# Kernel tuning notes

Hardware: AMD Instinct MI355X
Metric: run time of the kernel (lower is better)

The kernel has to match this reference:

```python
import math
import jax, jax.numpy as jnp
import numpy as np

ALPHA = 1000.0
N_LAMBDA = 1.0


def setup_inputs() -> dict:
    key = jax.random.key(0)
    k1, k2 = jax.random.split(key)
    xyz1 = jax.random.normal(k1, (4, 8192, 3), dtype=jnp.float32)  # prediction
    xyz2 = jax.random.normal(k2, (4, 8192, 3), dtype=jnp.float32)  # ground truth
    return {"xyz1": xyz1, "xyz2": xyz2}


def _nn(a, b):
    """For each point in a [B,Na,3], squared dist + index of nearest point in b [B,Nb,3]."""
    a2 = jnp.sum(a * a, axis=-1)[:, :, None]          # [B,Na,1]
    b2 = jnp.sum(b * b, axis=-1)[:, None, :]          # [B,1,Nb]
    d = a2 + b2 - 2.0 * jnp.einsum('bnd,bmd->bnm', a, b)  # [B,Na,Nb]
    return jnp.min(d, axis=-1), jnp.argmin(d, axis=-1)


def reference(xyz1, xyz2):
    B, n_x, _ = xyz1.shape
    n_gt = xyz2.shape[1]
    frac_21 = n_gt / n_x

    # torch code calls ChamferFunction.apply(xyz2, xyz1):
    # dist1/idx1 are for gt points (idx1 indexes into xyz1, range n_x),
    # dist2/idx2 are for pred points (idx2 indexes into xyz2, range n_gt).
    dist1, idx1 = _nn(xyz2, xyz1)   # [B, n_gt]
    dist2, idx2 = _nn(xyz1, xyz2)   # [B, n_x]

    exp_dist1 = jnp.exp(-dist1 * ALPHA)
    exp_dist2 = jnp.exp(-dist2 * ALPHA)

    batch = jnp.arange(B)[:, None]

    # how many gt points picked each pred point
    count1 = jnp.zeros((B, n_x), jnp.int32).at[batch, idx1].add(1)
    weight1 = jnp.take_along_axis(count1, idx1, axis=1).astype(jnp.float32) ** N_LAMBDA
    weight1 = 1.0 / jnp.maximum(frac_21 / weight1 + 1e-6, 1.0)
    loss1 = jnp.mean(1.0 - exp_dist1 * weight1, axis=1)

    # how many pred points picked each gt point
    count2 = jnp.zeros((B, n_gt), jnp.int32).at[batch, idx2].add(1)
    weight2 = jnp.take_along_axis(count2, idx2, axis=1).astype(jnp.float32) ** N_LAMBDA
    weight2 = 1.0 / (math.ceil(frac_21) * weight2 + 1e-6)
    loss2 = jnp.mean(1.0 - exp_dist2 * weight2, axis=1)

    return jnp.mean((loss1 + loss2) / 2.0)
```

## Files before the change

### kernel.cpp

```cpp
#include <hip/hip_runtime.h>
#include <cstdint>
#include <cstddef>

#define BATCH 4
#define NPTS 8192
#define CHUNK 128
#define BLOCK 256
#define QPT 8
#define QPB (BLOCK * QPT)
#define NKEYS (2 * BATCH * NPTS)

typedef float v2f __attribute__((ext_vector_type(2)));

__device__ __forceinline__ float halfnorm(float px, float py, float pz) {
    return 0.5f * fmaf(pz, pz, fmaf(py, py, px * px));
}
__device__ __forceinline__ float score(float qx, float qy, float qz,
                                       float px, float py, float pz, float ph) {
    float t = fmaf(-qx, px, ph);
    t = fmaf(-qy, py, t);
    return fmaf(-qz, pz, t);
}
__device__ __forceinline__ unsigned int mono_f32(float f) {
    unsigned int u = __float_as_uint(f);
    return u ^ (unsigned int)(((int)u >> 31) | 0x80000000);
}

__global__ void __launch_bounds__(BLOCK) prep_kernel(
        const float* __restrict__ xyz1,
        const float* __restrict__ xyz2,
        float* __restrict__ planes,
        unsigned int* __restrict__ counts,
        float* __restrict__ esum,
        float* __restrict__ out) {
    const int gtid = blockIdx.x * BLOCK + threadIdx.x;
    const int arr = gtid >> 15;
    const int rem = gtid & 32767;
    const int b = rem >> 13;
    const int i = rem & (NPTS - 1);
    const float* src = ((arr == 0) ? xyz1 : xyz2) + (size_t)(b * NPTS + i) * 3;
    const float px = src[0], py = src[1], pz = src[2];
    const size_t gb = ((size_t)(arr * 4 + b)) * 4 * NPTS;
    planes[gb + 0 * NPTS + i] = px;
    planes[gb + 1 * NPTS + i] = py;
    planes[gb + 2 * NPTS + i] = pz;
    planes[gb + 3 * NPTS + i] = halfnorm(px, py, pz);
    counts[gtid] = 0u;
    esum[gtid]   = 0.0f;
    if (gtid == 0) out[0] = 1.0f;
}

__global__ void __launch_bounds__(BLOCK, 4) nn_kernel(
        const float* __restrict__ xyz1,
        const float* __restrict__ xyz2,
        const float* __restrict__ planes,
        unsigned long long* __restrict__ keys) {
    const int tid = threadIdx.x;
    const int qt  = blockIdx.x;
    const int ct  = blockIdx.y;
    const int zb  = blockIdx.z;
    const int b   = zb & 3;
    const int dir = zb >> 2;
    const float* q_ptr = (dir == 0) ? xyz2 : xyz1;
    const int g = (dir == 0) ? b : 4 + b;
    const int chunk0 = ct * CHUNK;

    const float* Xp = planes + ((size_t)g * 4 + 0) * NPTS + chunk0;
    const float* Yp = planes + ((size_t)g * 4 + 1) * NPTS + chunk0;
    const float* Zp = planes + ((size_t)g * 4 + 2) * NPTS + chunk0;
    const float* Hp = planes + ((size_t)g * 4 + 3) * NPTS + chunk0;

    const int qbase = qt * QPB + tid;
    float qx[QPT], qy[QPT], qz[QPT];
#pragma unroll
    for (int u = 0; u < QPT; ++u) {
        const float* qp = q_ptr + (size_t)(b * NPTS + qbase + u * BLOCK) * 3;
        qx[u] = qp[0]; qy[u] = qp[1]; qz[u] = qp[2];
    }

    float bd[QPT];
    int   bj[QPT];
#pragma unroll
    for (int u = 0; u < QPT; ++u) { bd[u] = 3.4e38f; bj[u] = 0; }

#pragma unroll 2
    for (int j = 0; j < CHUNK; j += 8) {
        const v2f x01 = *(const v2f*)(Xp + j);
        const v2f x23 = *(const v2f*)(Xp + j + 2);
        const v2f x45 = *(const v2f*)(Xp + j + 4);
        const v2f x67 = *(const v2f*)(Xp + j + 6);
        const v2f y01 = *(const v2f*)(Yp + j);
        const v2f y23 = *(const v2f*)(Yp + j + 2);
        const v2f y45 = *(const v2f*)(Yp + j + 4);
        const v2f y67 = *(const v2f*)(Yp + j + 6);
        const v2f z01 = *(const v2f*)(Zp + j);
        const v2f z23 = *(const v2f*)(Zp + j + 2);
        const v2f z45 = *(const v2f*)(Zp + j + 4);
        const v2f z67 = *(const v2f*)(Zp + j + 6);
        const v2f h01 = *(const v2f*)(Hp + j);
        const v2f h23 = *(const v2f*)(Hp + j + 2);
        const v2f h45 = *(const v2f*)(Hp + j + 4);
        const v2f h67 = *(const v2f*)(Hp + j + 6);

#pragma unroll
        for (int u = 0; u < QPT; ++u) {
            const v2f nqx = {-qx[u], -qx[u]};
            const v2f nqy = {-qy[u], -qy[u]};
            const v2f nqz = {-qz[u], -qz[u]};
            v2f s01 = __builtin_elementwise_fma(nqx, x01, h01);
            v2f s23 = __builtin_elementwise_fma(nqx, x23, h23);
            v2f s45 = __builtin_elementwise_fma(nqx, x45, h45);
            v2f s67 = __builtin_elementwise_fma(nqx, x67, h67);
            s01 = __builtin_elementwise_fma(nqy, y01, s01);
            s23 = __builtin_elementwise_fma(nqy, y23, s23);
            s45 = __builtin_elementwise_fma(nqy, y45, s45);
            s67 = __builtin_elementwise_fma(nqy, y67, s67);
            s01 = __builtin_elementwise_fma(nqz, z01, s01);
            s23 = __builtin_elementwise_fma(nqz, z23, s23);
            s45 = __builtin_elementwise_fma(nqz, z45, s45);
            s67 = __builtin_elementwise_fma(nqz, z67, s67);

            float m0 = fminf(fminf(s01.x, s01.y), s23.x);
            float m1 = fminf(fminf(s23.y, s45.x), s45.y);
            float m2 = fminf(fminf(s67.x, s67.y), m0);
            float m  = fminf(m1, m2);
            if (m < bd[u]) { bd[u] = m; bj[u] = j; }
        }
    }

    const size_t base = ((size_t)zb) * NPTS;
#pragma unroll
    for (int u = 0; u < QPT; ++u) {
        unsigned long long key =
            ((unsigned long long)mono_f32(bd[u]) << 32) |
            (unsigned int)(chunk0 + bj[u]);
        atomicMin(&keys[base + qbase + u * BLOCK], key);
    }
}

__global__ void __launch_bounds__(BLOCK) mid_kernel(
        const float* __restrict__ xyz1,
        const float* __restrict__ xyz2,
        const unsigned long long* __restrict__ keys,
        unsigned int* __restrict__ counts,
        float* __restrict__ esum) {
    const int gtid = blockIdx.x * BLOCK + threadIdx.x;
    const int group = gtid >> 13;
    const int q   = gtid & (NPTS - 1);
    const int b   = group & 3;
    const int dir = group >> 2;
    const float* q_ptr = (dir == 0) ? xyz2 : xyz1;
    const float* d_ptr = (dir == 0) ? xyz1 : xyz2;

    const unsigned long long key = keys[gtid];
    const unsigned int smin_m = (unsigned int)(key >> 32);
    const int gbase = ((int)(unsigned int)key) & (NPTS - 8);

    const float* qp = q_ptr + (size_t)(b * NPTS + q) * 3;
    const float qx = qp[0], qy = qp[1], qz = qp[2];

    const float4* g4 = (const float4*)(d_ptr + (size_t)(b * NPTS + gbase) * 3);
    float4 t0 = g4[0], t1 = g4[1], t2 = g4[2], t3 = g4[3], t4 = g4[4], t5 = g4[5];
    float px[8] = {t0.x, t0.w, t1.z, t2.y, t3.x, t3.w, t4.z, t5.y};
    float py[8] = {t0.y, t1.x, t1.w, t2.z, t3.y, t4.x, t4.w, t5.z};
    float pz[8] = {t0.z, t1.y, t2.x, t2.w, t3.z, t4.y, t5.x, t5.w};

    int r = 0;
    float sx = px[0], sy = py[0], sz = pz[0];
#pragma unroll
    for (int k = 7; k >= 0; --k) {
        float ph = halfnorm(px[k], py[k], pz[k]);
        float s  = score(qx, qy, qz, px[k], py[k], pz[k], ph);
        if (mono_f32(s) == smin_m) { r = k; sx = px[k]; sy = py[k]; sz = pz[k]; }
    }
    const int idx = gbase + r;

    const float dx = qx - sx, dy = qy - sy, dz = qz - sz;
    const float d = dx * dx + dy * dy + dz * dz;
    const float e = expf(-1000.0f * d);

    atomicAdd(&counts[(size_t)group * NPTS + idx], 1u);
    atomicAdd(&esum[(size_t)group * NPTS + idx], e);
}

__global__ void __launch_bounds__(BLOCK) final_kernel(
        const unsigned int* __restrict__ counts,
        const float* __restrict__ esum,
        float* __restrict__ out) {
    __shared__ float red[4];
    const int gtid = blockIdx.x * BLOCK + threadIdx.x;
    const int dir = gtid >> 15;

    const float c = (float)counts[gtid];
    const float e = esum[gtid];
    float w;
    if (dir == 0) w = 1.0f / fmaxf(1.0f / c + 1e-6f, 1.0f);
    else          w = 1.0f / (c + 1e-6f);
    float term = -w * e;

#pragma unroll
    for (int off = 32; off > 0; off >>= 1)
        term += __shfl_down(term, off);
    const int lane = threadIdx.x & 63;
    const int wid  = threadIdx.x >> 6;
    if (lane == 0) red[wid] = term;
    __syncthreads();
    if (threadIdx.x == 0) {
        float t = red[0] + red[1] + red[2] + red[3];
        atomicAdd(out, t * (1.0f / 65536.0f));
    }
}

extern "C" void kernel_launch(void* const* d_in, const int* in_sizes, int n_in,
                              void* d_out, int out_size, void* d_ws, size_t ws_size,
                              hipStream_t stream) {
    const float* xyz1 = (const float*)d_in[0];
    const float* xyz2 = (const float*)d_in[1];
    float* out = (float*)d_out;

    unsigned long long* keys = (unsigned long long*)d_ws;
    unsigned int* counts = (unsigned int*)((char*)d_ws + (size_t)NKEYS * 8);
    float* esum = (float*)((char*)d_ws + (size_t)NKEYS * 12);
    float* planes = (float*)((char*)d_ws + (size_t)NKEYS * 16);

    prep_kernel<<<NKEYS / BLOCK, BLOCK, 0, stream>>>(xyz1, xyz2, planes,
                                                     counts, esum, out);
    nn_kernel<<<dim3(NPTS / QPB, NPTS / CHUNK, 2 * BATCH), BLOCK, 0, stream>>>(
        xyz1, xyz2, planes, keys);
    mid_kernel<<<NKEYS / BLOCK, BLOCK, 0, stream>>>(xyz1, xyz2, keys, counts, esum);
    final_kernel<<<NKEYS / BLOCK, BLOCK, 0, stream>>>(counts, esum, out);
}
```

Baseline: 109.5 us.

## Compute nearest-neighbour scores with split-bf16 MFMA and refine candidates in fp32

The packed-FMA distance scan is replaced by 32x32x16 bf16 MFMA instructions. Each coordinate and half-norm is split into hi and lo bf16 parts, so one MFMA gives a near-fp32 score for a 32x32 tile, and database chunks are staged in LDS. The nn kernel now records only the best 32-wide tile and 4-wide half, and the mid kernel rescans 16 candidates with exact fp32 distances to pick the index. This trades VALU work for matrix-core throughput, at the risk that the reduced precision of the split representation picks a different tile than exact fp32 in near-tie cases.

```diff
diff --git a/kernel.cpp b/kernel.cpp
--- a/kernel.cpp
+++ b/kernel.cpp
@@ -4,32 +4,33 @@
 
 #define BATCH 4
 #define NPTS 8192
-#define CHUNK 128
 #define BLOCK 256
-#define QPT 8
-#define QPB (BLOCK * QPT)
 #define NKEYS (2 * BATCH * NPTS)
-
-typedef float v2f __attribute__((ext_vector_type(2)));
+#define CHUNK_M 1024
+#define NTILES (CHUNK_M / 32)
+#define QPB 128
+
+
+typedef __attribute__((ext_vector_type(8))) short bf16x8;
+typedef __attribute__((ext_vector_type(16))) float f32x16;
 
 __device__ __forceinline__ float halfnorm(float px, float py, float pz) {
     return 0.5f * fmaf(pz, pz, fmaf(py, py, px * px));
-}
-__device__ __forceinline__ float score(float qx, float qy, float qz,
-                                       float px, float py, float pz, float ph) {
-    float t = fmaf(-qx, px, ph);
-    t = fmaf(-qy, py, t);
-    return fmaf(-qz, pz, t);
 }
 __device__ __forceinline__ unsigned int mono_f32(float f) {
     unsigned int u = __float_as_uint(f);
     return u ^ (unsigned int)(((int)u >> 31) | 0x80000000);
 }
+__device__ __forceinline__ unsigned int bf16_rne(float f) {
+    unsigned int u = __float_as_uint(f);
+    u = u + 0x7FFFu + ((u >> 16) & 1u);
+    return u >> 16;
+}
 
 __global__ void __launch_bounds__(BLOCK) prep_kernel(
         const float* __restrict__ xyz1,
         const float* __restrict__ xyz2,
-        float* __restrict__ planes,
+        uint4* __restrict__ planes,
         unsigned int* __restrict__ counts,
         float* __restrict__ esum,
         float* __restrict__ out) {
@@ -40,101 +41,98 @@
     const int i = rem & (NPTS - 1);
     const float* src = ((arr == 0) ? xyz1 : xyz2) + (size_t)(b * NPTS + i) * 3;
     const float px = src[0], py = src[1], pz = src[2];
-    const size_t gb = ((size_t)(arr * 4 + b)) * 4 * NPTS;
-    planes[gb + 0 * NPTS + i] = px;
-    planes[gb + 1 * NPTS + i] = py;
-    planes[gb + 2 * NPTS + i] = pz;
-    planes[gb + 3 * NPTS + i] = halfnorm(px, py, pz);
+    const float ph = halfnorm(px, py, pz);
+
+    const unsigned xh = bf16_rne(px);
+    const unsigned xl = bf16_rne(px - __uint_as_float(xh << 16));
+    const unsigned yh = bf16_rne(py);
+    const unsigned yl = bf16_rne(py - __uint_as_float(yh << 16));
+    const unsigned zh = bf16_rne(pz);
+    const unsigned zl = bf16_rne(pz - __uint_as_float(zh << 16));
+    const unsigned hh = bf16_rne(ph);
+    const unsigned hl = bf16_rne(ph - __uint_as_float(hh << 16));
+
+    uint4 w;
+    w.x = xh | (yh << 16);
+    w.y = zh | (xl << 16);
+    w.z = yl | (zl << 16);
+    w.w = hh | (hl << 16);
+    planes[(size_t)(arr * 4 + b) * NPTS + i] = w;
+
     counts[gtid] = 0u;
     esum[gtid]   = 0.0f;
     if (gtid == 0) out[0] = 1.0f;
 }
 
 __global__ void __launch_bounds__(BLOCK, 4) nn_kernel(
-        const float* __restrict__ xyz1,
-        const float* __restrict__ xyz2,
-        const float* __restrict__ planes,
+        const uint4* __restrict__ planes,
         unsigned long long* __restrict__ keys) {
+    __shared__ uint4 Alds[CHUNK_M];
     const int tid = threadIdx.x;
-    const int qt  = blockIdx.x;
-    const int ct  = blockIdx.y;
-    const int zb  = blockIdx.z;
-    const int b   = zb & 3;
+    const int wav = tid >> 6;
+    const int lane = tid & 63;
+    const int col = lane & 31;
+    const int h = lane >> 5;
+    const int qt = blockIdx.x;
+    const int ct = blockIdx.y;
+    const int zb = blockIdx.z;
+    const int b = zb & 3;
     const int dir = zb >> 2;
-    const float* q_ptr = (dir == 0) ? xyz2 : xyz1;
-    const int g = (dir == 0) ? b : 4 + b;
-    const int chunk0 = ct * CHUNK;
-
-    const float* Xp = planes + ((size_t)g * 4 + 0) * NPTS + chunk0;
-    const float* Yp = planes + ((size_t)g * 4 + 1) * NPTS + chunk0;
-    const float* Zp = planes + ((size_t)g * 4 + 2) * NPTS + chunk0;
-    const float* Hp = planes + ((size_t)g * 4 + 3) * NPTS + chunk0;
-
-    const int qbase = qt * QPB + tid;
-    float qx[QPT], qy[QPT], qz[QPT];
-#pragma unroll
-    for (int u = 0; u < QPT; ++u) {
-        const float* qp = q_ptr + (size_t)(b * NPTS + qbase + u * BLOCK) * 3;
-        qx[u] = qp[0]; qy[u] = qp[1]; qz[u] = qp[2];
-    }
-
-    float bd[QPT];
-    int   bj[QPT];
-#pragma unroll
-    for (int u = 0; u < QPT; ++u) { bd[u] = 3.4e38f; bj[u] = 0; }
-
+    const int g_db = (dir == 0) ? b : 4 + b;
+    const int g_q  = (dir == 0) ? 4 + b : b;
+
+    const uint4* asrc = planes + (size_t)g_db * NPTS + ct * CHUNK_M;
+#pragma unroll
+    for (int it = 0; it < CHUNK_M / BLOCK; ++it)
+        Alds[it * BLOCK + tid] = asrc[it * BLOCK + tid];
+
+    const int qidx = qt * QPB + wav * 32 + col;
+    const uint4 qw = planes[(size_t)g_q * NPTS + qidx];
+    unsigned b0, b1, b2, b3;
+    if (h == 0) {
+        const unsigned n0 = qw.x ^ 0x80008000u;
+        b0 = n0;
+        b1 = ((qw.y ^ 0x8000u) & 0xFFFFu) | (n0 << 16);
+        b2 = (n0 >> 16) | ((qw.y ^ 0x8000u) << 16);
+        b3 = 0x3F803F80u;
+    } else {
+        b0 = ((qw.y >> 16) | (qw.z << 16)) ^ 0x80008000u;
+        b1 = (qw.z >> 16) ^ 0x8000u;
+        b2 = 0u;
+        b3 = 0u;
+    }
+    uint4 bw; bw.x = b0; bw.y = b1; bw.z = b2; bw.w = b3;
+    const bf16x8 bf = __builtin_bit_cast(bf16x8, bw);
+    const f32x16 zacc = {};
+
+    __syncthreads();
+
+    float bd = 3.4e38f;
+    int bt = 0;
 #pragma unroll 2
-    for (int j = 0; j < CHUNK; j += 8) {
-        const v2f x01 = *(const v2f*)(Xp + j);
-        const v2f x23 = *(const v2f*)(Xp + j + 2);
-        const v2f x45 = *(const v2f*)(Xp + j + 4);
-        const v2f x67 = *(const v2f*)(Xp + j + 6);
-        const v2f y01 = *(const v2f*)(Yp + j);
-        const v2f y23 = *(const v2f*)(Yp + j + 2);
-        const v2f y45 = *(const v2f*)(Yp + j + 4);
-        const v2f y67 = *(const v2f*)(Yp + j + 6);
-        const v2f z01 = *(const v2f*)(Zp + j);
-        const v2f z23 = *(const v2f*)(Zp + j + 2);
-        const v2f z45 = *(const v2f*)(Zp + j + 4);
-        const v2f z67 = *(const v2f*)(Zp + j + 6);
-        const v2f h01 = *(const v2f*)(Hp + j);
-        const v2f h23 = *(const v2f*)(Hp + j + 2);
-        const v2f h45 = *(const v2f*)(Hp + j + 4);
-        const v2f h67 = *(const v2f*)(Hp + j + 6);
-
-#pragma unroll
-        for (int u = 0; u < QPT; ++u) {
-            const v2f nqx = {-qx[u], -qx[u]};
-            const v2f nqy = {-qy[u], -qy[u]};
-            const v2f nqz = {-qz[u], -qz[u]};
-            v2f s01 = __builtin_elementwise_fma(nqx, x01, h01);
-            v2f s23 = __builtin_elementwise_fma(nqx, x23, h23);
-            v2f s45 = __builtin_elementwise_fma(nqx, x45, h45);
-            v2f s67 = __builtin_elementwise_fma(nqx, x67, h67);
-            s01 = __builtin_elementwise_fma(nqy, y01, s01);
-            s23 = __builtin_elementwise_fma(nqy, y23, s23);
-            s45 = __builtin_elementwise_fma(nqy, y45, s45);
-            s67 = __builtin_elementwise_fma(nqy, y67, s67);
-            s01 = __builtin_elementwise_fma(nqz, z01, s01);
-            s23 = __builtin_elementwise_fma(nqz, z23, s23);
-            s45 = __builtin_elementwise_fma(nqz, z45, s45);
-            s67 = __builtin_elementwise_fma(nqz, z67, s67);
-
-            float m0 = fminf(fminf(s01.x, s01.y), s23.x);
-            float m1 = fminf(fminf(s23.y, s45.x), s45.y);
-            float m2 = fminf(fminf(s67.x, s67.y), m0);
-            float m  = fminf(m1, m2);
-            if (m < bd[u]) { bd[u] = m; bj[u] = j; }
-        }
-    }
-
-    const size_t base = ((size_t)zb) * NPTS;
-#pragma unroll
-    for (int u = 0; u < QPT; ++u) {
-        unsigned long long key =
-            ((unsigned long long)mono_f32(bd[u]) << 32) |
-            (unsigned int)(chunk0 + bj[u]);
-        atomicMin(&keys[base + qbase + u * BLOCK], key);
+    for (int t = 0; t < NTILES; ++t) {
+        const uint4 aw = Alds[t * 32 + col];
+        const bf16x8 af = __builtin_bit_cast(bf16x8, aw);
+        const f32x16 s =
+            __builtin_amdgcn_mfma_f32_32x32x16_bf16(af, bf, zacc, 0, 0, 0);
+        float m0 = fminf(fminf(s[0], s[1]), s[2]);
+        float m1 = fminf(fminf(s[3], s[4]), s[5]);
+        float m2 = fminf(fminf(s[6], s[7]), s[8]);
+        float m3 = fminf(fminf(s[9], s[10]), s[11]);
+        float m4 = fminf(fminf(s[12], s[13]), s[14]);
+        float m5 = fminf(fminf(s[15], m0), m1);
+        float m6 = fminf(fminf(m2, m3), m4);
+        const float m = fminf(m5, m6);
+        if (m < bd) { bd = m; bt = t; }
+    }
+
+    unsigned long long key =
+        ((unsigned long long)mono_f32(bd) << 32) |
+        (unsigned)(ct * CHUNK_M + (bt << 5) + (h << 2));
+    const unsigned long long other = __shfl_down(key, 32);
+    if (h == 0) {
+        if (other < key) key = other;
+        atomicMin(&keys[(size_t)zb * NPTS + qidx], key);
     }
 }
 
@@ -153,34 +151,32 @@
     const float* d_ptr = (dir == 0) ? xyz1 : xyz2;
 
     const unsigned long long key = keys[gtid];
-    const unsigned int smin_m = (unsigned int)(key >> 32);
-    const int gbase = ((int)(unsigned int)key) & (NPTS - 8);
+    const int base = ((int)(unsigned int)key) & ((NPTS - 32) | 4);
 
     const float* qp = q_ptr + (size_t)(b * NPTS + q) * 3;
     const float qx = qp[0], qy = qp[1], qz = qp[2];
 
-    const float4* g4 = (const float4*)(d_ptr + (size_t)(b * NPTS + gbase) * 3);
-    float4 t0 = g4[0], t1 = g4[1], t2 = g4[2], t3 = g4[3], t4 = g4[4], t5 = g4[5];
-    float px[8] = {t0.x, t0.w, t1.z, t2.y, t3.x, t3.w, t4.z, t5.y};
-    float py[8] = {t0.y, t1.x, t1.w, t2.z, t3.y, t4.x, t4.w, t5.z};
-    float pz[8] = {t0.z, t1.y, t2.x, t2.w, t3.z, t4.y, t5.x, t5.w};
-
-    int r = 0;
-    float sx = px[0], sy = py[0], sz = pz[0];
-#pragma unroll
-    for (int k = 7; k >= 0; --k) {
-        float ph = halfnorm(px[k], py[k], pz[k]);
-        float s  = score(qx, qy, qz, px[k], py[k], pz[k], ph);
-        if (mono_f32(s) == smin_m) { r = k; sx = px[k]; sy = py[k]; sz = pz[k]; }
-    }
-    const int idx = gbase + r;
-
-    const float dx = qx - sx, dy = qy - sy, dz = qz - sz;
-    const float d = dx * dx + dy * dy + dz * dz;
-    const float e = expf(-1000.0f * d);
-
-    atomicAdd(&counts[(size_t)group * NPTS + idx], 1u);
-    atomicAdd(&esum[(size_t)group * NPTS + idx], e);
+    float bestd = 3.4e38f;
+    int bestr = 0;
+#pragma unroll
+    for (int j = 0; j < 4; ++j) {
+        const int r0 = base + 8 * j;
+        const float4* g4 = (const float4*)(d_ptr + (size_t)(b * NPTS + r0) * 3);
+        const float4 t0 = g4[0], t1 = g4[1], t2 = g4[2];
+        const float px[4] = {t0.x, t0.w, t1.z, t2.y};
+        const float py[4] = {t0.y, t1.x, t1.w, t2.z};
+        const float pz[4] = {t0.z, t1.y, t2.x, t2.w};
+#pragma unroll
+        for (int k = 0; k < 4; ++k) {
+            const float dx = qx - px[k], dy = qy - py[k], dz = qz - pz[k];
+            const float d = dx * dx + dy * dy + dz * dz;
+            if (d < bestd) { bestd = d; bestr = r0 + k; }
+        }
+    }
+
+    const float e = expf(-1000.0f * bestd);
+    atomicAdd(&counts[(size_t)group * NPTS + bestr], 1u);
+    atomicAdd(&esum[(size_t)group * NPTS + bestr], e);
 }
 
 __global__ void __launch_bounds__(BLOCK) final_kernel(
@@ -221,12 +217,12 @@
     unsigned long long* keys = (unsigned long long*)d_ws;
     unsigned int* counts = (unsigned int*)((char*)d_ws + (size_t)NKEYS * 8);
     float* esum = (float*)((char*)d_ws + (size_t)NKEYS * 12);
-    float* planes = (float*)((char*)d_ws + (size_t)NKEYS * 16);
+    uint4* planes = (uint4*)((char*)d_ws + (size_t)NKEYS * 16);
 
     prep_kernel<<<NKEYS / BLOCK, BLOCK, 0, stream>>>(xyz1, xyz2, planes,
                                                      counts, esum, out);
-    nn_kernel<<<dim3(NPTS / QPB, NPTS / CHUNK, 2 * BATCH), BLOCK, 0, stream>>>(
-        xyz1, xyz2, planes, keys);
+    nn_kernel<<<dim3(NPTS / QPB, NPTS / CHUNK_M, 2 * BATCH), BLOCK, 0, stream>>>(
+        planes, keys);
     mid_kernel<<<NKEYS / BLOCK, BLOCK, 0, stream>>>(xyz1, xyz2, keys, counts, esum);
     final_kernel<<<NKEYS / BLOCK, BLOCK, 0, stream>>>(counts, esum, out);
 }
```

New measurement: 89.95 us. 17.8% less time.
